# Kernel tuning notes

Measured on AMD Instinct MI355X. Metric: run time of the kernel, lower is better.

The kernel has to match this reference:

```python
import jax, jax.numpy as jnp
import numpy as np

L2_IDX = np.array([0, 1, 2, 4, 24, 26, 35, 38])
S = 16    # n_scalar_features
H = 32    # hidden multiplicity
NL2 = 9   # number of 2e inputs (8 selected kernels + kernel sum)
B = 131072
NK = 40   # n_kernels


def _w3j_222():
    """Wigner 3j / CG tensor for 2e x 2e -> 2e in the real spherical-harmonic
    basis, Frobenius-normalized (e3nn convention up to an overall sign).
    Computed as the 1-D null space of the infinitesimal equivariance constraint."""
    l = 2
    mv = np.arange(-l, l + 1)
    Jp = np.zeros((5, 5), complex)
    for i, m in enumerate(mv[:-1]):
        Jp[i + 1, i] = np.sqrt(l * (l + 1) - m * (m + 1))
    Jm = Jp.conj().T
    Jx, Jy, Jz = (Jp + Jm) / 2, (Jp - Jm) / 2j, np.diag(mv).astype(complex)
    # complex -> real spherical harmonics change of basis
    Q = np.zeros((5, 5), complex)
    for m in mv:
        i = m + l
        if m < 0:
            Q[i, i] = 1j / np.sqrt(2)
            Q[i, l - m] = -1j * (-1.0) ** m / np.sqrt(2)
        elif m == 0:
            Q[i, i] = 1.0
        else:
            Q[i, l - m] = 1 / np.sqrt(2)
            Q[i, i] = (-1.0) ** m / np.sqrt(2)
    Gs = [np.real(-1j * Q @ J @ Q.conj().T) for J in (Jx, Jy, Jz)]  # real so(3) generators
    I5, I25 = np.eye(5), np.eye(25)
    M = np.concatenate([np.kron(G, I25) + np.kron(I5, np.kron(G, I5)) + np.kron(I25, G)
                        for G in Gs], axis=0)
    c = np.linalg.svd(M)[2][-1].reshape(5, 5, 5)
    c = c / np.linalg.norm(c)
    if c.flat[np.argmax(np.abs(c))] < 0:
        c = -c
    return c.astype(np.float32)


C222 = jnp.asarray(_w3j_222())
INV_SQRT5 = float(1.0 / np.sqrt(5.0))  # CG value for l,l->0 and 0,l->l paths


def setup_inputs() -> dict:
    key = jax.random.key(0)
    ks = jax.random.split(key, 10)
    return {
        "scalars": jax.random.normal(ks[0], (B, S), jnp.float32),
        "kernel_t2s": jax.random.normal(ks[1], (B, NK, 5), jnp.float32),
        "w000": jax.random.normal(ks[2], (S, S, H), jnp.float32),
        "w110": jax.random.normal(ks[3], (NL2, NL2, H), jnp.float32),
        "w011": jax.random.normal(ks[4], (S, NL2, H), jnp.float32),
        "w101": jax.random.normal(ks[5], (NL2, S, H), jnp.float32),
        "w111": jax.random.normal(ks[6], (NL2, NL2, H), jnp.float32),
        "v010": jax.random.normal(ks[7], (H, H), jnp.float32),
        "v100": jax.random.normal(ks[8], (H, H), jnp.float32),
        "v110": jax.random.normal(ks[9], (H, H), jnp.float32),
    }


def reference(scalars, kernel_t2s, w000, w110, w011, w101, w111, v010, v100, v110):
    s = scalars                                                  # (B, S)   0e inputs
    t = jnp.concatenate([kernel_t2s[:, L2_IDX, :],
                         kernel_t2s.sum(axis=1, keepdims=True)], axis=1)  # (B, 9, 5) 2e inputs

    # e3nn path-normalization coefficients (component / element defaults)
    c0 = (1.0 / (S * S + NL2 * NL2 * 5)) ** 0.5   # 0e out: fan-in S*S + 9*9*... -> S^2 + 81
    c0 = (1.0 / (S * S + 81)) ** 0.5
    c2 = (5.0 / (18 * S + 81)) ** 0.5             # 2e out: fan-in 9S + 9S + 81

    # ---- tp1(x, x): hidden = Hx0e + Hx2e ----
    h0 = c0 * (jnp.einsum('uvw,bu,bv->bw', w000, s, s)
               + INV_SQRT5 * jnp.einsum('uvw,bui,bvi->bw', w110, t, t))          # (B, H)
    u1 = jnp.einsum('bui,ijk->bujk', t, C222)                                    # (B,9,5,5)
    u2 = jnp.einsum('bujk,bvj->buvk', u1, t)                                     # (B,9,9,5)
    h2 = c2 * (INV_SQRT5 * jnp.einsum('uvw,bu,bvk->bwk', w011, s, t)
               + INV_SQRT5 * jnp.einsum('uvw,bui,bv->bwi', w101, t, s)
               + jnp.einsum('buvk,uvw->bwk', u2, w111))                          # (B, H, 5)

    # ---- tp2(h, h): 1x2e ----
    d = (5.0 / (3 * H * H)) ** 0.5
    a = jnp.einsum('uv,bvj->buj', v110, h2)       # (B, H, 5)
    b2 = jnp.einsum('bui,buj->bij', h2, a)        # (B, 5, 5)
    out = d * (INV_SQRT5 * (jnp.einsum('uv,bu,bvk->bk', v010, h0, h2)
                            + jnp.einsum('uv,buk,bv->bk', v100, h2, h0))
               + jnp.einsum('bij,ijk->bk', b2, C222))                            # (B, 5)
    return out
```

## Files before the change

### kernel.cpp

```cpp
#include <hip/hip_runtime.h>
#include <cmath>


#define DEVINL static __device__ __forceinline__

typedef _Float16 half2_t __attribute__((ext_vector_type(2)));
typedef _Float16 half8_t __attribute__((ext_vector_type(8)));
typedef float    f32x4_t __attribute__((ext_vector_type(4)));
union H8 { half8_t v; half2_t p[4]; };

#define FW0   0
#define FWC   6144
#define FMR   10752
#define FW111 11776
#define FV110 13824
#define SLABH 14848

__device__ __align__(16) _Float16 g_wsh[SLABH];

struct CPack { float v[32]; };

static constexpr int CIa[32] = {2,2,2,4,2,4,4,4, 2,0,0, 2,1,1, 2,3,3, 4,0,0, 4,1,1, 4,3,3, 0,0,1,1,3,3};
static constexpr int CJa[32] = {2,2,4,2,4,2,4,4, 0,2,0, 1,2,1, 3,2,3, 0,4,0, 1,4,1, 3,4,3, 1,3,0,3,0,1};
static constexpr int CKa[32] = {2,4,2,2,4,4,2,4, 0,0,2, 1,1,2, 3,3,2, 0,0,4, 1,1,4, 3,3,4, 3,1,3,0,1,0};

__host__ __device__ inline void tri_uv(int p, int n, int& u, int& v) {
  int base = 0;
  for (int x = 0; x < n; x++) {
    int c = n - x;
    if (p < base + c) { u = x; v = x + (p - base); return; }
    base += c;
  }
  u = n - 1; v = n - 1;
}

static double h_trE3(const double A[3][3], const double B[3][3], const double C[3][3]) {
  double t = 0.0;
  for (int r = 0; r < 3; r++)
    for (int c = 0; c < 3; c++) {
      double ab = 0.0;
      for (int m = 0; m < 3; m++) ab += A[r][m] * B[m][c];
      t += ab * C[c][r];
    }
  return t;
}
static void computeC(CPack& out) {
  const double s2i = 0.7071067811865475244, s6i = 0.4082482904638630164;
  double E[5][3][3] = {
    {{0, s2i, 0}, {s2i, 0, 0}, {0, 0, 0}},
    {{0, 0, 0}, {0, 0, s2i}, {0, s2i, 0}},
    {{-s6i, 0, 0}, {0, -s6i, 0}, {0, 0, 2.0 * s6i}},
    {{0, 0, s2i}, {0, 0, 0}, {s2i, 0, 0}},
    {{s2i, 0, 0}, {0, -s2i, 0}, {0, 0, 0}}
  };
  double T[125], nrm = 0.0;
  for (int f = 0; f < 125; f++) {
    int i = f / 25, j = (f / 5) % 5, k = f % 5;
    T[f] = h_trE3(E[i], E[j], E[k]) + h_trE3(E[i], E[k], E[j]);
    nrm += T[f] * T[f];
  }
  nrm = std::sqrt(nrm);
  int am = 0; double mx = std::fabs(T[0]);
  for (int q = 1; q < 125; q++) { double v = std::fabs(T[q]); if (v > mx) { mx = v; am = q; } }
  const double scale = ((T[am] < 0.0) ? 1.0 : -1.0) / nrm;
  for (int s = 0; s < 32; s++)
    out.v[s] = (float)(scale * T[(CIa[s] * 5 + CJa[s]) * 5 + CKa[s]]);
}

DEVINL float dot2f(half2_t a, half2_t b, float c) {
#if __has_builtin(__builtin_amdgcn_fdot2)
  return __builtin_amdgcn_fdot2(a, b, c, false);
#else
  return fmaf((float)a[0], (float)b[0], fmaf((float)a[1], (float)b[1], c));
#endif
}
DEVINL half2_t pk2(float a, float b) {
  auto r = __builtin_amdgcn_cvt_pkrtz(a, b);
  half2_t o;
  __builtin_memcpy(&o, &r, sizeof(o));
  return o;
}
DEVINL int h2i(half2_t h) { int i; __builtin_memcpy(&i, &h, 4); return i; }
DEVINL half2_t i2h(int i) { half2_t h; __builtin_memcpy(&h, &i, 4); return h; }
DEVINL f32x4_t mfma16(half8_t a, half8_t b, f32x4_t c) {
  return __builtin_amdgcn_mfma_f32_16x16x32_f16(a, b, c, 0, 0, 0);
}
DEVINL void store4h(_Float16* p, f32x4_t d) {
  int2 v;
  v.x = h2i(pk2(d[0], d[1]));
  v.y = h2i(pk2(d[2], d[3]));
  *(int2*)p = v;
}

DEVINL void bar_lds() {
  asm volatile("s_waitcnt lgkmcnt(0)" ::: "memory");
  __builtin_amdgcn_s_barrier();
  __builtin_amdgcn_sched_barrier(0);
}

__global__ void ech_setup(const float* __restrict__ w000, const float* __restrict__ w110,
                          const float* __restrict__ w011, const float* __restrict__ w101,
                          const float* __restrict__ w111, const float* __restrict__ v010,
                          const float* __restrict__ v100, const float* __restrict__ v110) {
  const float c0   = 1.0f / sqrtf(337.0f);
  const float inv5 = 0.44721359549995794f;
  const float c2   = sqrtf(5.0f / 369.0f);
  const float dm   = sqrtf(5.0f / 3072.0f) * inv5;
  int gid = blockIdx.x * blockDim.x + threadIdx.x;
  int gs  = gridDim.x * blockDim.x;

  for (int idx = gid; idx < 6144; idx += gs) {
    int j = idx & 7, L = (idx >> 3) & 63, tk = idx >> 9;
    int mt = tk / 6, ks = tk % 6;
    int w = mt * 16 + (L & 15);
    int p = ks * 32 + (L >> 4) * 8 + j;
    float x = 0.0f;
    if (p < 136) {
      int u, v; tri_uv(p, 16, u, v);
      x = c0 * (w000[(u * 16 + v) * 32 + w] + (u != v ? w000[(v * 16 + u) * 32 + w] : 0.0f));
    } else if (p < 181) {
      int u, v; tri_uv(p - 136, 9, u, v);
      x = c0 * inv5 * (w110[(u * 9 + v) * 32 + w] + (u != v ? w110[(v * 9 + u) * 32 + w] : 0.0f));
    }
    g_wsh[FW0 + idx] = (_Float16)x;
  }
  for (int idx = gid; idx < 4608; idx += gs) {
    int j = idx & 7, L = (idx >> 3) & 31, t = idx >> 8;
    int m = t * 16 + (L & 15);
    int w = m / 9, v = m % 9;
    int u = (L >> 4) * 8 + j;
    g_wsh[FWC + idx] =
        (_Float16)(c2 * inv5 * (w011[(u * 9 + v) * 32 + w] + w101[(v * 16 + u) * 32 + w]));
  }
  for (int idx = gid; idx < 1024; idx += gs) {
    int j = idx & 7, L = (idx >> 3) & 63, mt = idx >> 9;
    int w = mt * 16 + (L & 15);
    int u = (L >> 4) * 8 + j;
    g_wsh[FMR + idx] = (_Float16)(dm * (v010[u * 32 + w] + v100[w * 32 + u]));
  }
  for (int idx = gid; idx < 2048; idx += gs) {
    int j = idx & 7, L = (idx >> 3) & 63, t = idx >> 9;
    int mt = t >> 1, ks = t & 1;
    int w = mt * 16 + (L & 15);
    int p = ks * 32 + (L >> 4) * 8 + j;
    float x = 0.0f;
    if (p < 45) { int u, v; tri_uv(p, 9, u, v);
      x = c2 * (w111[(u * 9 + v) * 32 + w] + (u != v ? w111[(v * 9 + u) * 32 + w] : 0.0f)); }
    g_wsh[FW111 + idx] = (_Float16)x;
  }
  for (int idx = gid; idx < 1024; idx += gs) {
    int j = idx & 7, L = (idx >> 3) & 63, mt = idx >> 9;
    int u = mt * 16 + (L & 15);
    int v = (L >> 4) * 8 + j;
    g_wsh[FV110 + idx] = (_Float16)v110[u * 32 + v];
  }
}

#define ESZ 444
#define P5MT 272
#define P5K  544
__global__ void __launch_bounds__(512)
ech_main(const float* __restrict__ sc, const float* __restrict__ t2s,
         float* __restrict__ out, int nGroups, CPack C) {
  __shared__ __align__(16) _Float16 slabh[SLABH];
  __shared__ __align__(16) float scr[16 * ESZ];
  __shared__ __align__(16) _Float16 unionH[5280];
  __shared__ __align__(16) _Float16 cvvH[16 * 288];
  __shared__ __align__(16) _Float16 h0st[16 * 40];
  __shared__ __align__(16) _Float16 gst[16 * 40];
  __shared__ int pairs9[48];
  __shared__ int sspair[68];

  const int tid  = threadIdx.x;
  const int lane = tid & 31;
  const int sub  = tid >> 5;
  const int w    = lane;

  _Float16* p5H  = unionH;
  _Float16* h2Bb = unionH + 2720;

  for (int i = tid; i < SLABH / 8; i += 512)
    ((float4*)slabh)[i] = ((const float4*)g_wsh)[i];
  if (tid < 45) { int u, v; tri_uv(tid, 9, u, v); pairs9[tid] = u | (v << 4); }
  if (tid < 68) {
    int u0, v0, u1, v1;
    tri_uv(2 * tid, 16, u0, v0);
    tri_uv(2 * tid + 1, 16, u1, v1);
    sspair[tid] = u0 | (v0 << 4) | (u1 << 8) | (v1 << 12);
  }

  constexpr int L2R[8] = {0, 1, 2, 4, 24, 26, 35, 38};

  float*     E    = scr + sub * ESZ;
  float*     Araw = E;
  _Float16*  qBe  = (_Float16*)E;
  float*     tb   = E + 200;
  _Float16*  sshh = (_Float16*)(E + 272);
  _Float16*  tthh = (_Float16*)(E + 340);
  _Float16*  thh  = (_Float16*)(E + 368);
  float*     sL   = E + 408;
  int*       spad = (int*)(E + 424);

  if (lane < 11)      tthh[45 + lane] = (_Float16)0.f;
  else if (lane < 16) thh[(lane - 11) * 16 + 9] = (_Float16)0.f;
  if (lane >= 24)     spad[lane - 16] = 0;

  float4 pf0 = {0.f, 0.f, 0.f, 0.f};
  float4 pf1 = {0.f, 0.f, 0.f, 0.f};
  float4 pfs = {0.f, 0.f, 0.f, 0.f};
  if (blockIdx.x < nGroups) {
    const int b0 = blockIdx.x * 16 + sub;
    const float4* src = (const float4*)(t2s + (size_t)b0 * 200);
    pf0 = src[lane];
    if (lane < 18) pf1 = src[lane + 32];
    if (lane < 4)  pfs = ((const float4*)(sc + (size_t)b0 * 16))[lane];
  }
  __syncthreads();

  for (int grp = blockIdx.x; grp < nGroups; grp += gridDim.x) {
    const int b = grp * 16 + sub;

    {
      float4* Av = (float4*)Araw;
      Av[lane] = pf0;
      if (lane < 18) Av[lane + 32] = pf1;
      if (lane < 4) ((float4*)sL)[lane] = pfs;
    }
    {
      const int gnext = grp + gridDim.x;
      if (gnext < nGroups) {
        const int bn = gnext * 16 + sub;
        const float4* srcn = (const float4*)(t2s + (size_t)bn * 200);
        pf0 = srcn[lane];
        if (lane < 18) pf1 = srcn[lane + 32];
        if (lane < 4)  pfs = ((const float4*)(sc + (size_t)bn * 16))[lane];
      }
    }
    if (lane < 8) spad[lane] = h2i(pk2(sL[2 * lane], sL[2 * lane + 1]));

    #pragma unroll
    for (int it = 0; it < 2; it++) {
      int idx = lane + 32 * it;
      if (idx < 40) {
        int r = idx / 5, c = idx % 5;
        float val = Araw[L2R[r] * 5 + c];
        tb[r * 8 + c] = val;
        thh[c * 16 + r] = (_Float16)val;
      }
    }
    {
      int l25 = lane % 25;
      int c2 = l25 / 5, j2 = l25 % 5;
      float acc = 0.f;
      #pragma unroll
      for (int rr = 0; rr < 8; rr++) acc += Araw[(j2 + 5 * rr) * 5 + c2];
      float tot = __shfl(acc, 5 * c2 + 0, 32) + __shfl(acc, 5 * c2 + 1, 32)
                + __shfl(acc, 5 * c2 + 2, 32) + __shfl(acc, 5 * c2 + 3, 32)
                + __shfl(acc, 5 * c2 + 4, 32);
      if (lane < 25 && j2 == 0) { tb[64 + c2] = tot; thh[c2 * 16 + 8] = (_Float16)tot; }
    }

    #pragma unroll
    for (int it = 0; it < 2; it++) {
      int idx = lane + 32 * it;
      if (idx < 45) {
        int pr = pairs9[idx];
        int pu = pr & 15, pv = pr >> 4;
        float4 u4 = *(const float4*)(tb + pu * 8); float u5 = tb[pu * 8 + 4];
        float4 v4 = *(const float4*)(tb + pv * 8); float v5 = tb[pv * 8 + 4];
        float tu[5] = {u4.x, u4.y, u4.z, u4.w, u5};
        float tv[5] = {v4.x, v4.y, v4.z, v4.w, v5};
        float tt = tu[0]*tv[0] + tu[1]*tv[1] + tu[2]*tv[2] + tu[3]*tv[3] + tu[4]*tv[4];
        tthh[idx] = (_Float16)tt;
        float qk[5] = {0, 0, 0, 0, 0};
        #pragma unroll
        for (int s = 0; s < 32; s++)
          qk[CKa[s]] = fmaf(C.v[s], tu[CIa[s]] * tv[CJa[s]], qk[CKa[s]]);
        #pragma unroll
        for (int k = 0; k < 5; k++) qBe[k * 64 + idx] = (_Float16)qk[k];
      } else {
        #pragma unroll
        for (int k = 0; k < 5; k++) qBe[k * 64 + idx] = (_Float16)0.f;
      }
    }

    #pragma unroll
    for (int ii = 0; ii < 3; ii++) {
      int slot = lane + 32 * ii;
      if (slot < 68) {
        int t = sspair[slot];
        int u0 = t & 15, v0 = (t >> 4) & 15, u1 = (t >> 8) & 15, v1 = (t >> 12) & 15;
        *(half2_t*)(sshh + 2 * slot) = pk2(sL[u0] * sL[v0], sL[u1] * sL[v1]);
      }
    }
    bar_lds();

    {
      const int wid = tid >> 6;
      const int L   = tid & 63;
      const int e2  = L & 15;
      const int q2  = L >> 4;
      const _Float16* scrH = (const _Float16*)scr;
      if (wid == 0) {
        f32x4_t a0 = {0.f, 0.f, 0.f, 0.f}, a1 = {0.f, 0.f, 0.f, 0.f};
        const _Float16* ssb = scrH + e2 * (2 * ESZ) + 544;
        #pragma unroll
        for (int ks = 0; ks < 6; ks++) {
          half8_t bb = *(const half8_t*)(ssb + ks * 32 + q2 * 8);
          a0 = mfma16(*(const half8_t*)(slabh + FW0 + ks * 512 + L * 8), bb, a0);
          a1 = mfma16(*(const half8_t*)(slabh + FW0 + (6 + ks) * 512 + L * 8), bb, a1);
        }
        store4h(h0st + e2 * 40 + q2 * 4, a0);
        store4h(h0st + e2 * 40 + 16 + q2 * 4, a1);
      } else if (wid <= 2) {
        const _Float16* spb = scrH + e2 * (2 * ESZ) + 848;
        half8_t bb = *(const half8_t*)(spb + q2 * 8);
        const int t0 = (wid - 1) * 9;
        half8_t wz = {0, 0, 0, 0, 0, 0, 0, 0};
        #pragma unroll
        for (int t = 0; t < 9; t++) {
          half8_t wa = (q2 < 2) ? *(const half8_t*)(slabh + FWC + (t0 + t) * 256 + L * 8) : wz;
          f32x4_t z4 = {0.f, 0.f, 0.f, 0.f};
          f32x4_t d = mfma16(wa, bb, z4);
          store4h(cvvH + e2 * 288 + (t0 + t) * 16 + q2 * 4, d);
        }
      } else {
        const int k = wid - 3;
        const _Float16* qb = scrH + e2 * (2 * ESZ) + k * 64;
        f32x4_t d0 = {0.f, 0.f, 0.f, 0.f}, d1 = {0.f, 0.f, 0.f, 0.f};
        #pragma unroll
        for (int ks = 0; ks < 2; ks++) {
          half8_t bb = *(const half8_t*)(qb + ks * 32 + q2 * 8);
          d0 = mfma16(*(const half8_t*)(slabh + FW111 + ks * 512 + L * 8), bb, d0);
          d1 = mfma16(*(const half8_t*)(slabh + FW111 + (2 + ks) * 512 + L * 8), bb, d1);
        }
        store4h(p5H + k * P5K + e2 * 16 + q2 * 4, d0);
        store4h(p5H + k * P5K + P5MT + e2 * 16 + q2 * 4, d1);
      }
    }
    bar_lds();

    float Cvv[9];
    #pragma unroll
    for (int v = 0; v < 9; v++) Cvv[v] = (float)cvvH[sub * 288 + w * 9 + v];
    half2_t cpk[5] = { pk2(Cvv[0], Cvv[1]), pk2(Cvv[2], Cvv[3]),
                       pk2(Cvv[4], Cvv[5]), pk2(Cvv[6], Cvv[7]), pk2(Cvv[8], 0.f) };
    float h2r[5];
    #pragma unroll
    for (int k = 0; k < 5; k++) {
      H8 d; d.v = *(const half8_t*)(thh + k * 16);
      half2_t d4 = *(const half2_t*)(thh + k * 16 + 8);
      float acc = dot2f(cpk[0], d.p[0], 0.f);
      acc = dot2f(cpk[1], d.p[1], acc);
      acc = dot2f(cpk[2], d.p[2], acc);
      acc = dot2f(cpk[3], d.p[3], acc);
      acc = dot2f(cpk[4], d4, acc);
      h2r[k] = acc + (float)p5H[k * P5K + (w >> 4) * P5MT + sub * 16 + (w & 15)];
    }
    #pragma unroll
    for (int k = 0; k < 5; k++) h2Bb[k * 512 + sub * 32 + w] = (_Float16)h2r[k];
    bar_lds();

    {
      const int wid = tid >> 6;
      const int L   = tid & 63;
      const int e2  = L & 15;
      const int q2  = L >> 4;
      if (wid < 5) {
        const int j = wid;
        half8_t bb = *(const half8_t*)(h2Bb + j * 512 + e2 * 32 + q2 * 8);
        f32x4_t z4 = {0.f, 0.f, 0.f, 0.f};
        f32x4_t d0 = mfma16(*(const half8_t*)(slabh + FV110 + L * 8), bb, z4);
        f32x4_t d1 = mfma16(*(const half8_t*)(slabh + FV110 + 512 + L * 8), bb, z4);
        store4h(p5H + j * P5K + e2 * 16 + q2 * 4, d0);
        store4h(p5H + j * P5K + P5MT + e2 * 16 + q2 * 4, d1);
      } else if (wid == 5) {
        half8_t hb = *(const half8_t*)(h0st + e2 * 40 + q2 * 8);
        f32x4_t z4 = {0.f, 0.f, 0.f, 0.f};
        f32x4_t g0 = mfma16(*(const half8_t*)(slabh + FMR + L * 8), hb, z4);
        f32x4_t g1 = mfma16(*(const half8_t*)(slabh + FMR + 512 + L * 8), hb, z4);
        store4h(gst + e2 * 40 + q2 * 4, g0);
        store4h(gst + e2 * 40 + 16 + q2 * 4, g1);
      }
    }
    bar_lds();

    float a5[5];
    #pragma unroll
    for (int j = 0; j < 5; j++)
      a5[j] = (float)p5H[j * P5K + (w >> 4) * P5MT + sub * 16 + (w & 15)];
    float g = (float)gst[sub * 40 + w];

    float yv[5] = {0, 0, 0, 0, 0};
    #pragma unroll
    for (int s = 0; s < 32; s++)
      yv[CKa[s]] = fmaf(C.v[s], h2r[CIa[s]] * a5[CJa[s]], yv[CKa[s]]);

    const float DCONST = sqrtf(5.0f / 3072.0f);
    float z[5];
    #pragma unroll
    for (int k = 0; k < 5; k++) z[k] = fmaf(DCONST, yv[k], g * h2r[k]);

    half2_t z01 = pk2(z[0], z[1]);
    half2_t z23 = pk2(z[2], z[3]);
    float   z4r = z[4];
    #pragma unroll
    for (int st = 1; st <= 16; st <<= 1) {
      z01 = z01 + i2h(__shfl_xor(h2i(z01), st));
      z23 = z23 + i2h(__shfl_xor(h2i(z23), st));
      z4r += __shfl_xor(z4r, st);
    }
    if (lane < 5) {
      float val = (lane == 0) ? (float)z01[0]
                : (lane == 1) ? (float)z01[1]
                : (lane == 2) ? (float)z23[0]
                : (lane == 3) ? (float)z23[1] : z4r;
      out[(size_t)b * 5 + lane] = val;
    }
  }
}

extern "C" void kernel_launch(void* const* d_in, const int* in_sizes, int n_in,
                              void* d_out, int out_size, void* d_ws, size_t ws_size,
                              hipStream_t stream) {
  (void)n_in; (void)out_size; (void)d_ws; (void)ws_size;

  CPack C;
  computeC(C);

  ech_setup<<<64, 256, 0, stream>>>(
      (const float*)d_in[2], (const float*)d_in[3], (const float*)d_in[4],
      (const float*)d_in[5], (const float*)d_in[6], (const float*)d_in[7],
      (const float*)d_in[8], (const float*)d_in[9]);

  const int B = in_sizes[0] / 16;
  const int nGroups = B / 16;
  ech_main<<<512, 512, 0, stream>>>(
      (const float*)d_in[0], (const float*)d_in[1], (float*)d_out, nGroups, C);
}
```

Before: 242.7 us.

## Drop LDS weight slab, load MFMA weights from global, size grid by occupancy

Removes the per-block shared-memory copy of the half-precision weight slab and has each wave load its MFMA A-fragments directly from global (L2-cached) memory into registers. This frees roughly 30 KB of LDS per block so more blocks can be resident per CU, and launch bounds now request 6 blocks. The grid is sized from a queried occupancy times 256 CUs instead of a fixed 512 blocks. The cost is repeated global or L2 weight loads in every group iteration and higher register pressure from holding the fragments in VGPRs.

```diff
diff --git a/kernel.cpp b/kernel.cpp
--- a/kernel.cpp
+++ b/kernel.cpp
@@ -159,10 +159,9 @@
 #define ESZ 444
 #define P5MT 272
 #define P5K  544
-__global__ void __launch_bounds__(512)
+__global__ void __launch_bounds__(512, 6)
 ech_main(const float* __restrict__ sc, const float* __restrict__ t2s,
          float* __restrict__ out, int nGroups, CPack C) {
-  __shared__ __align__(16) _Float16 slabh[SLABH];
   __shared__ __align__(16) float scr[16 * ESZ];
   __shared__ __align__(16) _Float16 unionH[5280];
   __shared__ __align__(16) _Float16 cvvH[16 * 288];
@@ -179,8 +178,6 @@
   _Float16* p5H  = unionH;
   _Float16* h2Bb = unionH + 2720;
 
-  for (int i = tid; i < SLABH / 8; i += 512)
-    ((float4*)slabh)[i] = ((const float4*)g_wsh)[i];
   if (tid < 45) { int u, v; tri_uv(tid, 9, u, v); pairs9[tid] = u | (v << 4); }
   if (tid < 68) {
     int u0, v0, u1, v1;
@@ -302,13 +299,20 @@
       const int q2  = L >> 4;
       const _Float16* scrH = (const _Float16*)scr;
       if (wid == 0) {
+        const _Float16* fw = g_wsh + FW0 + (size_t)L * 8;
+        half8_t fA[6], fB[6];
+        #pragma unroll
+        for (int ks = 0; ks < 6; ks++) {
+          fA[ks] = *(const half8_t*)(fw + ks * 512);
+          fB[ks] = *(const half8_t*)(fw + (6 + ks) * 512);
+        }
         f32x4_t a0 = {0.f, 0.f, 0.f, 0.f}, a1 = {0.f, 0.f, 0.f, 0.f};
         const _Float16* ssb = scrH + e2 * (2 * ESZ) + 544;
         #pragma unroll
         for (int ks = 0; ks < 6; ks++) {
           half8_t bb = *(const half8_t*)(ssb + ks * 32 + q2 * 8);
-          a0 = mfma16(*(const half8_t*)(slabh + FW0 + ks * 512 + L * 8), bb, a0);
-          a1 = mfma16(*(const half8_t*)(slabh + FW0 + (6 + ks) * 512 + L * 8), bb, a1);
+          a0 = mfma16(fA[ks], bb, a0);
+          a1 = mfma16(fB[ks], bb, a1);
         }
         store4h(h0st + e2 * 40 + q2 * 4, a0);
         store4h(h0st + e2 * 40 + 16 + q2 * 4, a1);
@@ -319,20 +323,25 @@
         half8_t wz = {0, 0, 0, 0, 0, 0, 0, 0};
         #pragma unroll
         for (int t = 0; t < 9; t++) {
-          half8_t wa = (q2 < 2) ? *(const half8_t*)(slabh + FWC + (t0 + t) * 256 + L * 8) : wz;
+          half8_t wa = (q2 < 2)
+              ? *(const half8_t*)(g_wsh + FWC + (t0 + t) * 256 + (size_t)L * 8) : wz;
           f32x4_t z4 = {0.f, 0.f, 0.f, 0.f};
           f32x4_t d = mfma16(wa, bb, z4);
           store4h(cvvH + e2 * 288 + (t0 + t) * 16 + q2 * 4, d);
         }
       } else {
         const int k = wid - 3;
+        const _Float16* fw = g_wsh + FW111 + (size_t)L * 8;
+        half8_t fA[4];
+        #pragma unroll
+        for (int q = 0; q < 4; q++) fA[q] = *(const half8_t*)(fw + q * 512);
         const _Float16* qb = scrH + e2 * (2 * ESZ) + k * 64;
         f32x4_t d0 = {0.f, 0.f, 0.f, 0.f}, d1 = {0.f, 0.f, 0.f, 0.f};
         #pragma unroll
         for (int ks = 0; ks < 2; ks++) {
           half8_t bb = *(const half8_t*)(qb + ks * 32 + q2 * 8);
-          d0 = mfma16(*(const half8_t*)(slabh + FW111 + ks * 512 + L * 8), bb, d0);
-          d1 = mfma16(*(const half8_t*)(slabh + FW111 + (2 + ks) * 512 + L * 8), bb, d1);
+          d0 = mfma16(fA[ks], bb, d0);
+          d1 = mfma16(fA[2 + ks], bb, d1);
         }
         store4h(p5H + k * P5K + e2 * 16 + q2 * 4, d0);
         store4h(p5H + k * P5K + P5MT + e2 * 16 + q2 * 4, d1);
@@ -368,17 +377,23 @@
       const int q2  = L >> 4;
       if (wid < 5) {
         const int j = wid;
+        const _Float16* fw = g_wsh + FV110 + (size_t)L * 8;
+        half8_t f0 = *(const half8_t*)(fw);
+        half8_t f1 = *(const half8_t*)(fw + 512);
         half8_t bb = *(const half8_t*)(h2Bb + j * 512 + e2 * 32 + q2 * 8);
         f32x4_t z4 = {0.f, 0.f, 0.f, 0.f};
-        f32x4_t d0 = mfma16(*(const half8_t*)(slabh + FV110 + L * 8), bb, z4);
-        f32x4_t d1 = mfma16(*(const half8_t*)(slabh + FV110 + 512 + L * 8), bb, z4);
+        f32x4_t d0 = mfma16(f0, bb, z4);
+        f32x4_t d1 = mfma16(f1, bb, z4);
         store4h(p5H + j * P5K + e2 * 16 + q2 * 4, d0);
         store4h(p5H + j * P5K + P5MT + e2 * 16 + q2 * 4, d1);
       } else if (wid == 5) {
+        const _Float16* fw = g_wsh + FMR + (size_t)L * 8;
+        half8_t f0 = *(const half8_t*)(fw);
+        half8_t f1 = *(const half8_t*)(fw + 512);
         half8_t hb = *(const half8_t*)(h0st + e2 * 40 + q2 * 8);
         f32x4_t z4 = {0.f, 0.f, 0.f, 0.f};
-        f32x4_t g0 = mfma16(*(const half8_t*)(slabh + FMR + L * 8), hb, z4);
-        f32x4_t g1 = mfma16(*(const half8_t*)(slabh + FMR + 512 + L * 8), hb, z4);
+        f32x4_t g0 = mfma16(f0, hb, z4);
+        f32x4_t g1 = mfma16(f1, hb, z4);
         store4h(gst + e2 * 40 + q2 * 4, g0);
         store4h(gst + e2 * 40 + 16 + q2 * 4, g1);
       }
@@ -435,6 +450,17 @@
 
   const int B = in_sizes[0] / 16;
   const int nGroups = B / 16;
-  ech_main<<<512, 512, 0, stream>>>(
+
+  static int blocksPerCU = 0;
+  if (blocksPerCU == 0) {
+    int n = 0;
+    if (hipOccupancyMaxActiveBlocksPerMultiprocessor(&n, ech_main, 512, 0) != hipSuccess || n < 1)
+      n = 2;
+    blocksPerCU = n;
+  }
+  int grid = blocksPerCU * 256;
+  if (grid > nGroups) grid = nGroups;
+
+  ech_main<<<grid, 512, 0, stream>>>(
       (const float*)d_in[0], (const float*)d_in[1], (float*)d_out, nGroups, C);
 }
```

Measured after the change: 392.8 us. 61.9% more time.
